# Performance work log

Measured on AMD Instinct MI355X. Metric: run time of the kernel, lower is better.

The kernel has to match this reference:

```python
import jax, jax.numpy as jnp
import numpy as np

NEAR, FAR, N_SAMPLES = 0.5, 10.0, 128
B, R, C = 8, 16384, 3


def setup_inputs() -> dict:
    key = jax.random.key(0)
    k1, k2 = jax.random.split(key)
    sigmas = jax.random.normal(k1, (B, R, N_SAMPLES, 1), dtype=jnp.float32)
    radiances = jax.random.uniform(k2, (B, R, N_SAMPLES, C), dtype=jnp.float32)
    z_vals = jnp.linspace(NEAR, FAR, N_SAMPLES, dtype=jnp.float32)  # [Z]
    return {"sigmas": sigmas, "radiances": radiances, "z_vals": z_vals}


def reference(sigmas, radiances, z_vals):
    # dists: [Z], last interval repeated (as in torch code)
    d = z_vals[1:] - z_vals[:-1]
    dists = jnp.concatenate([d, d[-1:]], axis=-1)
    # alpha = 1 - exp(-relu(sigma) * dist)  -> [B,R,Z,1]
    alpha = 1.0 - jnp.exp(-jax.nn.relu(sigmas) * dists[None, None, :, None])
    # shifted transmittance: prepend ones along Z, cumprod of (1-alpha+eps)
    alpha_shifted = jnp.concatenate(
        [jnp.ones_like(alpha[:, :, :1]), 1.0 - alpha + 1e-10], axis=-2
    )
    Ts = jnp.cumprod(alpha_shifted, axis=-2)
    weights = alpha * Ts[..., :-1, :]  # [B,R,Z,1]
    # rgb: einsum('brzs,brzs->brs') with s-broadcast => weighted sum over Z
    rgb = jnp.sum(weights * radiances, axis=-2)  # [B,R,C]
    depth_map = jnp.sum(weights * z_vals[None, None, :, None], axis=-2)  # [B,R,1]
    return rgb, depth_map, weights
```

## Files before the change

### kernel.cpp

```cpp
#include <hip/hip_runtime.h>
#include <cstddef>

#define NSAMP 128
#define WAVES_PER_BLOCK 4

__global__ __launch_bounds__(256) void volrend_kernel(
    const float* __restrict__ sig,
    const float* __restrict__ rad,
    const float* __restrict__ zv,
    float* __restrict__ rgb,
    float* __restrict__ depth,
    float* __restrict__ wts,
    int n_rays)
{
    const int lane = threadIdx.x & 63;
    const int ray  = blockIdx.x * WAVES_PER_BLOCK + (threadIdx.x >> 6);
    if (ray >= n_rays) return;

    const int za = lane;
    const int zb = lane + 64;

    const float z_a = zv[za];
    const float z_b = zv[zb];
    const float dist_a = zv[za + 1] - z_a;
    const float dist_b = zv[min(zb + 1, 127)] - zv[min(zb, 126)];

    const float* sray = sig + (size_t)ray * NSAMP;
    const float sa = sray[za];
    const float sb = sray[zb];
    const float ea = expf(-fmaxf(sa, 0.0f) * dist_a);
    const float eb = expf(-fmaxf(sb, 0.0f) * dist_b);
    const float alpha_a = 1.0f - ea;
    const float alpha_b = 1.0f - eb;
    const float fa = ea + 1e-10f;
    const float fb = eb + 1e-10f;

    float p = fa;
    #pragma unroll
    for (int d = 1; d < 64; d <<= 1) {
        float t = __shfl_up(p, d);
        if (lane >= d) p *= t;
    }
    float Ta = __shfl_up(p, 1);
    if (lane == 0) Ta = 1.0f;
    const float Tfull = __shfl(p, 63);

    float q = fb;
    #pragma unroll
    for (int d = 1; d < 64; d <<= 1) {
        float t = __shfl_up(q, d);
        if (lane >= d) q *= t;
    }
    float Tb = __shfl_up(q, 1);
    Tb = (lane == 0) ? Tfull : Tb * Tfull;

    const float wa = alpha_a * Ta;
    const float wb = alpha_b * Tb;

    float* wray = wts + (size_t)ray * NSAMP;
    wray[za] = wa;
    wray[zb] = wb;

    const float* rray = rad + (size_t)ray * (NSAMP * 3);
    float s0 = wa * rray[3 * za + 0] + wb * rray[3 * zb + 0];
    float s1 = wa * rray[3 * za + 1] + wb * rray[3 * zb + 1];
    float s2 = wa * rray[3 * za + 2] + wb * rray[3 * zb + 2];
    float s3 = wa * z_a + wb * z_b;

    #pragma unroll
    for (int d = 32; d > 0; d >>= 1) {
        s0 += __shfl_xor(s0, d);
        s1 += __shfl_xor(s1, d);
        s2 += __shfl_xor(s2, d);
        s3 += __shfl_xor(s3, d);
    }
    if (lane == 0) {
        rgb[(size_t)ray * 3 + 0] = s0;
        rgb[(size_t)ray * 3 + 1] = s1;
        rgb[(size_t)ray * 3 + 2] = s2;
        depth[ray] = s3;
    }
}

extern "C" void kernel_launch(void* const* d_in, const int* in_sizes, int n_in,
                              void* d_out, int out_size, void* d_ws, size_t ws_size,
                              hipStream_t stream) {
    const float* sig = (const float*)d_in[0];
    const float* rad = (const float*)d_in[1];
    const float* zv  = (const float*)d_in[2];

    const int n_rays = in_sizes[0] / NSAMP;

    float* rgb   = (float*)d_out;
    float* depth = rgb + (size_t)n_rays * 3;
    float* wts   = depth + (size_t)n_rays;

    const int blocks = (n_rays + WAVES_PER_BLOCK - 1) / WAVES_PER_BLOCK;
    volrend_kernel<<<blocks, 64 * WAVES_PER_BLOCK, 0, stream>>>(
        sig, rad, zv, rgb, depth, wts, n_rays);
}
```

Before: 328.2 us.

## Vectorize ray loads via LDS staging, single scan over sample pairs, packed reductions

Each lane now owns two adjacent samples, so sigma, z and weights move as 2-wide vector accesses, and radiance is loaded coalesced with nontemporal 8-byte loads and staged through shared memory. One 64-lane product scan over pair products replaces the two scans. The final reduction folds the four sums into one lane-interleaved butterfly, cutting shuffle count. It also switches to fast __expf, adds a block barrier, and clamps out-of-range rays to the last ray instead of returning early.

```diff
diff --git a/kernel.cpp b/kernel.cpp
--- a/kernel.cpp
+++ b/kernel.cpp
@@ -2,7 +2,9 @@
 #include <cstddef>
 
 #define NSAMP 128
-#define WAVES_PER_BLOCK 4
+#define WPB 4
+
+typedef float f32x2 __attribute__((ext_vector_type(2)));
 
 __global__ __launch_bounds__(256) void volrend_kernel(
     const float* __restrict__ sig,
@@ -13,72 +15,79 @@
     float* __restrict__ wts,
     int n_rays)
 {
+    __shared__ float lds[WPB][384];
+
     const int lane = threadIdx.x & 63;
-    const int ray  = blockIdx.x * WAVES_PER_BLOCK + (threadIdx.x >> 6);
-    if (ray >= n_rays) return;
+    const int wid  = threadIdx.x >> 6;
+    int ray = blockIdx.x * WPB + wid;
+    if (ray >= n_rays) ray = n_rays - 1;
 
-    const int za = lane;
-    const int zb = lane + 64;
+    const int z0 = 2 * lane;
 
-    const float z_a = zv[za];
-    const float z_b = zv[zb];
-    const float dist_a = zv[za + 1] - z_a;
-    const float dist_b = zv[min(zb + 1, 127)] - zv[min(zb, 126)];
+    const f32x2* rrow = (const f32x2*)(rad + (size_t)ray * 384);
+    f32x2 r0 = __builtin_nontemporal_load(rrow + lane);
+    f32x2 r1 = __builtin_nontemporal_load(rrow + 64 + lane);
+    f32x2 r2 = __builtin_nontemporal_load(rrow + 128 + lane);
+    f32x2* lrow = (f32x2*)lds[wid];
+    lrow[lane]       = r0;
+    lrow[64 + lane]  = r1;
+    lrow[128 + lane] = r2;
 
-    const float* sray = sig + (size_t)ray * NSAMP;
-    const float sa = sray[za];
-    const float sb = sray[zb];
-    const float ea = expf(-fmaxf(sa, 0.0f) * dist_a);
-    const float eb = expf(-fmaxf(sb, 0.0f) * dist_b);
-    const float alpha_a = 1.0f - ea;
-    const float alpha_b = 1.0f - eb;
-    const float fa = ea + 1e-10f;
-    const float fb = eb + 1e-10f;
+    const f32x2 sv = __builtin_nontemporal_load(
+        (const f32x2*)(sig + (size_t)ray * NSAMP) + lane);
 
-    float p = fa;
+    const f32x2 z01 = *((const f32x2*)zv + lane);
+    const float z2  = zv[min(z0 + 2, 127)];
+    const float d0  = z01.y - z01.x;
+    const float d1  = (z0 + 1 < 127) ? (z2 - z01.y) : d0;
+
+    const float e0 = __expf(-fmaxf(sv.x, 0.0f) * d0);
+    const float e1 = __expf(-fmaxf(sv.y, 0.0f) * d1);
+    const float a0 = 1.0f - e0;
+    const float a1 = 1.0f - e1;
+    const float f0 = e0 + 1e-10f;
+    const float f1 = e1 + 1e-10f;
+
+    float p = f0 * f1;
     #pragma unroll
     for (int d = 1; d < 64; d <<= 1) {
         float t = __shfl_up(p, d);
         if (lane >= d) p *= t;
     }
-    float Ta = __shfl_up(p, 1);
-    if (lane == 0) Ta = 1.0f;
-    const float Tfull = __shfl(p, 63);
+    float E = __shfl_up(p, 1);
+    if (lane == 0) E = 1.0f;
 
-    float q = fb;
-    #pragma unroll
-    for (int d = 1; d < 64; d <<= 1) {
-        float t = __shfl_up(q, d);
-        if (lane >= d) q *= t;
-    }
-    float Tb = __shfl_up(q, 1);
-    Tb = (lane == 0) ? Tfull : Tb * Tfull;
+    const float w0 = a0 * E;
+    const float w1 = a1 * (E * f0);
 
-    const float wa = alpha_a * Ta;
-    const float wb = alpha_b * Tb;
+    f32x2 wv; wv.x = w0; wv.y = w1;
+    __builtin_nontemporal_store(wv, (f32x2*)(wts + (size_t)ray * NSAMP) + lane);
 
-    float* wray = wts + (size_t)ray * NSAMP;
-    wray[za] = wa;
-    wray[zb] = wb;
+    __syncthreads();
+    const float* lp = lds[wid] + 6 * lane;
+    float s0 = w0 * lp[0] + w1 * lp[3];
+    float s1 = w0 * lp[1] + w1 * lp[4];
+    float s2 = w0 * lp[2] + w1 * lp[5];
+    float s3 = w0 * z01.x + w1 * z01.y;
 
-    const float* rray = rad + (size_t)ray * (NSAMP * 3);
-    float s0 = wa * rray[3 * za + 0] + wb * rray[3 * zb + 0];
-    float s1 = wa * rray[3 * za + 1] + wb * rray[3 * zb + 1];
-    float s2 = wa * rray[3 * za + 2] + wb * rray[3 * zb + 2];
-    float s3 = wa * z_a + wb * z_b;
+    s0 += __shfl_xor(s0, 32);
+    s1 += __shfl_xor(s1, 32);
+    s2 += __shfl_xor(s2, 32);
+    s3 += __shfl_xor(s3, 32);
+    float A = (lane & 32) ? s2 : s0;
+    float B = (lane & 32) ? s3 : s1;
+    A += __shfl_xor(A, 16);
+    B += __shfl_xor(B, 16);
+    float v = (lane & 16) ? B : A;
+    v += __shfl_xor(v, 8);
+    v += __shfl_xor(v, 4);
+    v += __shfl_xor(v, 2);
+    v += __shfl_xor(v, 1);
 
-    #pragma unroll
-    for (int d = 32; d > 0; d >>= 1) {
-        s0 += __shfl_xor(s0, d);
-        s1 += __shfl_xor(s1, d);
-        s2 += __shfl_xor(s2, d);
-        s3 += __shfl_xor(s3, d);
-    }
-    if (lane == 0) {
-        rgb[(size_t)ray * 3 + 0] = s0;
-        rgb[(size_t)ray * 3 + 1] = s1;
-        rgb[(size_t)ray * 3 + 2] = s2;
-        depth[ray] = s3;
+    if ((lane & 15) == 0) {
+        const int c = lane >> 4;
+        if (c < 3) rgb[(size_t)ray * 3 + c] = v;
+        else       depth[ray] = v;
     }
 }
 
@@ -95,7 +104,7 @@
     float* depth = rgb + (size_t)n_rays * 3;
     float* wts   = depth + (size_t)n_rays;
 
-    const int blocks = (n_rays + WAVES_PER_BLOCK - 1) / WAVES_PER_BLOCK;
-    volrend_kernel<<<blocks, 64 * WAVES_PER_BLOCK, 0, stream>>>(
+    const int blocks = (n_rays + WPB - 1) / WPB;
+    volrend_kernel<<<blocks, 64 * WPB, 0, stream>>>(
         sig, rad, zv, rgb, depth, wts, n_rays);
 }
```

Measured after the change: 312.7 us. 4.7% less time.
